# Performance work log

Hardware: AMD Instinct MI355X
Metric: run time of the kernel (lower is better)

## Reference

```python
import jax, jax.numpy as jnp
import numpy as np

B = 65536
D = 8          # model dim (hard-wired in source)
H = 2          # num_heads
A = 20         # act_size
L = 5          # tokens per embedding stream


def _attn_layer(x, Wqkv, bqkv, Wo, bo, Wl, bl):
    # x: [B, S, D]
    Bx, S, Dx = x.shape
    hd = Dx // H
    qkv = x @ Wqkv.T + bqkv                      # [B, S, 3D]
    q, k, v = jnp.split(qkv, 3, axis=-1)
    def split_heads(t):
        return t.reshape(Bx, S, H, hd).transpose(0, 2, 1, 3)  # [B,H,S,hd]
    q, k, v = split_heads(q), split_heads(k), split_heads(v)
    scores = jnp.einsum('bhqd,bhkd->bhqk', q, k) * (hd ** -0.5)
    attn = jax.nn.softmax(scores, axis=-1)       # dropout inactive at eval
    o = jnp.einsum('bhqk,bhkd->bhqd', attn, v)
    o = o.transpose(0, 2, 1, 3).reshape(Bx, S, Dx)
    x = x + (o @ Wo.T + bo)                      # residual after attention
    h = jax.nn.relu(x @ Wl.T + bl)               # linear + relu
    return x + h                                 # second residual


def setup_inputs() -> dict:
    key = jax.random.key(0)
    ks = jax.random.split(key, 20)
    s = 1.0 / np.sqrt(D)
    inp = {
        'dice_type': jax.random.randint(ks[0], (B, L), 0, 15),
        'dice_star': jax.random.randint(ks[1], (B, L), 0, 15),
        'summon_lvl': jax.random.randint(ks[2], (B, L), 0, 2),
        'emb_dice': jax.random.normal(ks[3], (15, D), jnp.float32),
        'emb_star': jax.random.normal(ks[4], (15, D), jnp.float32),
        'emb_btns': jax.random.normal(ks[5], (2, D), jnp.float32),
        'Wout': jax.random.normal(ks[6], (A, D), jnp.float32) * s,
        'bout': jnp.zeros((A,), jnp.float32),
    }
    for i in range(2):
        o = 7 + 5 * i
        inp[f'Wqkv{i}'] = jax.random.normal(ks[o], (3 * D, D), jnp.float32) * s
        inp[f'bqkv{i}'] = jnp.zeros((3 * D,), jnp.float32)
        inp[f'Wo{i}'] = jax.random.normal(ks[o + 1], (D, D), jnp.float32) * s
        inp[f'bo{i}'] = jnp.zeros((D,), jnp.float32)
        inp[f'Wl{i}'] = jax.random.normal(ks[o + 2], (D, D), jnp.float32) * s
        inp[f'bl{i}'] = jnp.zeros((D,), jnp.float32)
    return inp


def reference(dice_type, dice_star, summon_lvl,
              emb_dice, emb_star, emb_btns,
              Wqkv0, bqkv0, Wo0, bo0, Wl0, bl0,
              Wqkv1, bqkv1, Wo1, bo1, Wl1, bl1,
              Wout, bout):
    x = jnp.concatenate([emb_dice[dice_type],
                         emb_star[dice_star],
                         emb_btns[summon_lvl]], axis=1)  # [B, 15, D]
    x = _attn_layer(x, Wqkv0, bqkv0, Wo0, bo0, Wl0, bl0)
    x = _attn_layer(x, Wqkv1, bqkv1, Wo1, bo1, Wl1, bl1)
    x = jnp.mean(x, axis=1)                               # [B, D]
    return x @ Wout.T + bout                              # [B, A]
```

## Files before the change

### kernel.cpp

```cpp
#include <hip/hip_runtime.h>
#include <math.h>

#define EPB 16
#define BTOT 65536
#define C_SCALE 0.72134752044f

typedef _Float16 h2 __attribute__((ext_vector_type(2)));

#define WQKV1 0
#define BQKV1 96
#define WO0   108
#define BO0   140
#define WL0   144
#define BL0   176
#define WO1   180
#define BO1   212
#define WL1   216
#define BL1   248

__device__ __forceinline__ float exp2_fast(float x) {
#if defined(__has_builtin)
#if __has_builtin(__builtin_amdgcn_exp2f)
  return __builtin_amdgcn_exp2f(x);
#else
  return exp2f(x);
#endif
#else
  return exp2f(x);
#endif
}

union F4H2 { float4 f; h2 h[4]; };

__device__ __forceinline__ void mm8_h2(const h2* __restrict__ wp, int woff, int boff,
                                       const h2 in2[4], h2 out2[4])
{
#pragma unroll
  for (int c2 = 0; c2 < 4; ++c2) {
    h2 acc = wp[boff + c2];
#pragma unroll
    for (int p = 0; p < 4; ++p) {
      acc += (h2)(in2[p].x) * wp[woff + c2 * 8 + 2 * p];
      acc += (h2)(in2[p].y) * wp[woff + c2 * 8 + 2 * p + 1];
    }
    out2[c2] = acc;
  }
}

__global__ void BetterBot_setup(const float* __restrict__ Wqkv1, const float* __restrict__ bqkv1,
                                const float* __restrict__ Wo0, const float* __restrict__ bo0,
                                const float* __restrict__ Wl0, const float* __restrict__ bl0,
                                const float* __restrict__ Wo1, const float* __restrict__ bo1,
                                const float* __restrict__ Wl1, const float* __restrict__ bl1,
                                h2* __restrict__ ws)
{
  const int tid = threadIdx.x;
  if (tid < 96) {
    const int c2 = tid >> 3, j = tid & 7;
    float a = Wqkv1[(2 * c2) * 8 + j], b = Wqkv1[(2 * c2 + 1) * 8 + j];
    if (c2 < 4) { a *= C_SCALE; b *= C_SCALE; }
    ws[tid] = (h2){(_Float16)a, (_Float16)b};
  } else if (tid < 108) {
    const int c2 = tid - 96;
    float a = bqkv1[2 * c2], b = bqkv1[2 * c2 + 1];
    if (c2 < 4) { a *= C_SCALE; b *= C_SCALE; }
    ws[tid] = (h2){(_Float16)a, (_Float16)b};
  } else if (tid < 140) {
    const int k = tid - 108, c2 = k >> 3, j = k & 7;
    ws[tid] = (h2){(_Float16)Wo0[(2 * c2) * 8 + j], (_Float16)Wo0[(2 * c2 + 1) * 8 + j]};
  } else if (tid < 144) {
    const int c2 = tid - 140;
    ws[tid] = (h2){(_Float16)bo0[2 * c2], (_Float16)bo0[2 * c2 + 1]};
  } else if (tid < 176) {
    const int k = tid - 144, c2 = k >> 3, j = k & 7;
    ws[tid] = (h2){(_Float16)Wl0[(2 * c2) * 8 + j], (_Float16)Wl0[(2 * c2 + 1) * 8 + j]};
  } else if (tid < 180) {
    const int c2 = tid - 176;
    ws[tid] = (h2){(_Float16)bl0[2 * c2], (_Float16)bl0[2 * c2 + 1]};
  } else if (tid < 212) {
    const int k = tid - 180, c2 = k >> 3, j = k & 7;
    ws[tid] = (h2){(_Float16)Wo1[(2 * c2) * 8 + j], (_Float16)Wo1[(2 * c2 + 1) * 8 + j]};
  } else if (tid < 216) {
    const int c2 = tid - 212;
    ws[tid] = (h2){(_Float16)bo1[2 * c2], (_Float16)bo1[2 * c2 + 1]};
  } else if (tid < 248) {
    const int k = tid - 216, c2 = k >> 3, j = k & 7;
    ws[tid] = (h2){(_Float16)Wl1[(2 * c2) * 8 + j], (_Float16)Wl1[(2 * c2 + 1) * 8 + j]};
  } else if (tid < 252) {
    const int c2 = tid - 248;
    ws[tid] = (h2){(_Float16)bl1[2 * c2], (_Float16)bl1[2 * c2 + 1]};
  }
}

__global__ __launch_bounds__(256, 4) void BetterBot_44169443672375_kernel(
    const int* __restrict__ dice_type, const int* __restrict__ dice_star,
    const int* __restrict__ summon_lvl,
    const float* __restrict__ emb_dice, const float* __restrict__ emb_star,
    const float* __restrict__ emb_btns,
    const float* __restrict__ Wout, const float* __restrict__ bout,
    const float* __restrict__ Wqkv0, const float* __restrict__ bqkv0,
    const h2* __restrict__ wp,
    float* __restrict__ out)
{
  __shared__ __align__(16) float qkT[32][20];
  __shared__ __align__(16) h2 vT[32][4];
  __shared__ __align__(16) h2 xT[32][4];
  __shared__ h2 eT[32 * 33];
  __shared__ int idxT[EPB][16];
  __shared__ __align__(16) float kvb[EPB][15][16];

  const int tid = threadIdx.x;
  const int e = tid >> 4;
  const int t = tid & 15;
  const int ge = blockIdx.x * EPB + e;

  int myc = 0;
  if (t < 15) {
    int c;
    if (t < 5)       c = dice_type[ge * 5 + t];
    else if (t < 10) c = 15 + dice_star[ge * 5 + (t - 5)];
    else             c = 30 + summon_lvl[ge * 5 + (t - 10)];
    idxT[e][t] = c;
    myc = c;
  }
  {
    const int c = tid >> 3;
    const int l8 = tid & 7;
    const float* er;
    if (c < 15)      er = emb_dice + 8 * c;
    else if (c < 30) er = emb_star + 8 * (c - 15);
    else             er = emb_btns + 8 * (c - 30);
    const float4 r0 = ((const float4*)er)[0];
    const float4 r1 = ((const float4*)er)[1];
    float r[8] = {r0.x, r0.y, r0.z, r0.w, r1.x, r1.y, r1.z, r1.w};
    if (l8 < 4) xT[c][l8] = (h2){(_Float16)r[2 * l8], (_Float16)r[2 * l8 + 1]};
    float aq = bqkv0[l8], ak = bqkv0[8 + l8], av = bqkv0[16 + l8];
#pragma unroll
    for (int j = 0; j < 8; ++j) {
      aq = fmaf(r[j], Wqkv0[l8 * 8 + j], aq);
      ak = fmaf(r[j], Wqkv0[(8 + l8) * 8 + j], ak);
      av = fmaf(r[j], Wqkv0[(16 + l8) * 8 + j], av);
    }
    qkT[c][l8] = aq * C_SCALE;
    qkT[c][8 + l8] = ak;
    const float vn = __shfl_xor(av, 1);
    if ((l8 & 1) == 0) vT[c][l8 >> 1] = (h2){(_Float16)av, (_Float16)vn};
  }
  __syncthreads();

  {
    const int qi = tid >> 3;
    const int ki0 = (tid & 7) * 4;
    float qv[8];
#pragma unroll
    for (int j = 0; j < 8; ++j) qv[j] = qkT[qi][j];
#pragma unroll
    for (int jj = 0; jj < 4; ++jj) {
      const int ki = ki0 + jj;
      const float* kr = &qkT[ki][8];
      float s0 = qv[0] * kr[0];
      s0 = fmaf(qv[1], kr[1], s0); s0 = fmaf(qv[2], kr[2], s0); s0 = fmaf(qv[3], kr[3], s0);
      float s1 = qv[4] * kr[4];
      s1 = fmaf(qv[5], kr[5], s1); s1 = fmaf(qv[6], kr[6], s1); s1 = fmaf(qv[7], kr[7], s1);
      eT[qi * 33 + ki] = (h2){(_Float16)exp2_fast(s0), (_Float16)exp2_fast(s1)};
    }
  }
  __syncthreads();

  h2 x2[4];
  float q1f[8];
  if (t < 15) {
    F4H2 xx; xx.f = *(const float4*)(&xT[myc][0]);
#pragma unroll
    for (int p = 0; p < 4; ++p) x2[p] = xx.h[p];

    h2 o2[4] = {(h2)(_Float16)0.f, (h2)(_Float16)0.f, (h2)(_Float16)0.f, (h2)(_Float16)0.f};
    float sum0 = 0.f, sum1 = 0.f;
    const h2* myE = eT + myc * 33;
#pragma unroll
    for (int u = 0; u < 15; ++u) {
      const int uc = idxT[e][u];
      const h2 ee = myE[uc];
      F4H2 vv; vv.f = *(const float4*)(&vT[uc][0]);
      const h2 el = (h2)(ee.x);
      const h2 eh = (h2)(ee.y);
      o2[0] += el * vv.h[0];
      o2[1] += el * vv.h[1];
      o2[2] += eh * vv.h[2];
      o2[3] += eh * vv.h[3];
      sum0 += (float)ee.x;
      sum1 += (float)ee.y;
    }
    const float r0 = 1.0f / sum0, r1 = 1.0f / sum1;
    o2[0] *= (h2)(_Float16)r0; o2[1] *= (h2)(_Float16)r0;
    o2[2] *= (h2)(_Float16)r1; o2[3] *= (h2)(_Float16)r1;

    h2 y2[4], xn2[4], hh2[4];
    mm8_h2(wp, WO0, BO0, o2, y2);
#pragma unroll
    for (int p = 0; p < 4; ++p) xn2[p] = x2[p] + y2[p];
    mm8_h2(wp, WL0, BL0, xn2, hh2);
    const h2 z2 = (h2)(_Float16)0.f;
#pragma unroll
    for (int p = 0; p < 4; ++p) x2[p] = xn2[p] + __builtin_elementwise_max(hh2[p], z2);

    h2 qkv2[12];
#pragma unroll
    for (int c2 = 0; c2 < 12; ++c2) {
      h2 acc = wp[BQKV1 + c2];
#pragma unroll
      for (int p = 0; p < 4; ++p) {
        acc += (h2)(x2[p].x) * wp[WQKV1 + c2 * 8 + 2 * p];
        acc += (h2)(x2[p].y) * wp[WQKV1 + c2 * 8 + 2 * p + 1];
      }
      qkv2[c2] = acc;
    }
#pragma unroll
    for (int p = 0; p < 4; ++p) {
      q1f[2 * p] = (float)qkv2[p].x;
      q1f[2 * p + 1] = (float)qkv2[p].y;
    }
    *(float4*)(&kvb[e][t][0]) = make_float4((float)qkv2[4].x, (float)qkv2[4].y,
                                            (float)qkv2[5].x, (float)qkv2[5].y);
    *(float4*)(&kvb[e][t][4]) = make_float4((float)qkv2[6].x, (float)qkv2[6].y,
                                            (float)qkv2[7].x, (float)qkv2[7].y);
    *(float4*)(&kvb[e][t][8]) = make_float4((float)qkv2[8].x, (float)qkv2[8].y,
                                            (float)qkv2[9].x, (float)qkv2[9].y);
    *(float4*)(&kvb[e][t][12]) = make_float4((float)qkv2[10].x, (float)qkv2[10].y,
                                             (float)qkv2[11].x, (float)qkv2[11].y);
  }
  __syncthreads();

  float xo[8] = {0.f, 0.f, 0.f, 0.f, 0.f, 0.f, 0.f, 0.f};
  if (t < 15) {
    float o[8] = {0.f, 0.f, 0.f, 0.f, 0.f, 0.f, 0.f, 0.f};
    float sum0 = 0.f, sum1 = 0.f;
#pragma unroll
    for (int u = 0; u < 15; ++u) {
      const float4 ka = *(const float4*)(&kvb[e][u][0]);
      const float4 kb2 = *(const float4*)(&kvb[e][u][4]);
      const float4 va = *(const float4*)(&kvb[e][u][8]);
      const float4 vb2 = *(const float4*)(&kvb[e][u][12]);
      float s0 = q1f[0] * ka.x;
      s0 = fmaf(q1f[1], ka.y, s0); s0 = fmaf(q1f[2], ka.z, s0); s0 = fmaf(q1f[3], ka.w, s0);
      float s1 = q1f[4] * kb2.x;
      s1 = fmaf(q1f[5], kb2.y, s1); s1 = fmaf(q1f[6], kb2.z, s1); s1 = fmaf(q1f[7], kb2.w, s1);
      const float e0 = exp2_fast(s0);
      const float e1 = exp2_fast(s1);
      sum0 += e0; sum1 += e1;
      o[0] = fmaf(e0, va.x, o[0]); o[1] = fmaf(e0, va.y, o[1]);
      o[2] = fmaf(e0, va.z, o[2]); o[3] = fmaf(e0, va.w, o[3]);
      o[4] = fmaf(e1, vb2.x, o[4]); o[5] = fmaf(e1, vb2.y, o[5]);
      o[6] = fmaf(e1, vb2.z, o[6]); o[7] = fmaf(e1, vb2.w, o[7]);
    }
    const float r0 = 1.0f / sum0, r1 = 1.0f / sum1;
    h2 po2[4];
    po2[0] = (h2){(_Float16)(o[0] * r0), (_Float16)(o[1] * r0)};
    po2[1] = (h2){(_Float16)(o[2] * r0), (_Float16)(o[3] * r0)};
    po2[2] = (h2){(_Float16)(o[4] * r1), (_Float16)(o[5] * r1)};
    po2[3] = (h2){(_Float16)(o[6] * r1), (_Float16)(o[7] * r1)};

    h2 y2[4], xn2[4], hh2[4];
    mm8_h2(wp, WO1, BO1, po2, y2);
#pragma unroll
    for (int p = 0; p < 4; ++p) xn2[p] = x2[p] + y2[p];
    mm8_h2(wp, WL1, BL1, xn2, hh2);
    const h2 z2 = (h2)(_Float16)0.f;
#pragma unroll
    for (int p = 0; p < 4; ++p) {
      const h2 xf = xn2[p] + __builtin_elementwise_max(hh2[p], z2);
      xo[2 * p] = (float)xf.x;
      xo[2 * p + 1] = (float)xf.y;
    }
  }

  float p[8];
#pragma unroll
  for (int j = 0; j < 8; ++j) p[j] = xo[j];
#pragma unroll
  for (int j = 0; j < 8; ++j) p[j] += __shfl_xor(p[j], 1);
#pragma unroll
  for (int j = 0; j < 8; ++j) p[j] += __shfl_xor(p[j], 2);
#pragma unroll
  for (int j = 0; j < 8; ++j) p[j] += __shfl_xor(p[j], 4);
#pragma unroll
  for (int j = 0; j < 8; ++j) p[j] += __shfl_xor(p[j], 8);
  float mean[8];
#pragma unroll
  for (int j = 0; j < 8; ++j) mean[j] = p[j] * (1.0f / 15.0f);

  const int obase = ge * 20;
  {
    float acc = bout[t];
#pragma unroll
    for (int j = 0; j < 8; ++j) acc = fmaf(mean[j], Wout[t * 8 + j], acc);
    out[obase + t] = acc;
  }
  if (t < 4) {
    const int a = 16 + t;
    float acc = bout[a];
#pragma unroll
    for (int j = 0; j < 8; ++j) acc = fmaf(mean[j], Wout[a * 8 + j], acc);
    out[obase + a] = acc;
  }
}

extern "C" void kernel_launch(void* const* d_in, const int* in_sizes, int n_in,
                              void* d_out, int out_size, void* d_ws, size_t ws_size,
                              hipStream_t stream) {
  const int*   dice_type  = (const int*)d_in[0];
  const int*   dice_star  = (const int*)d_in[1];
  const int*   summon_lvl = (const int*)d_in[2];
  const float* emb_dice   = (const float*)d_in[3];
  const float* emb_star   = (const float*)d_in[4];
  const float* emb_btns   = (const float*)d_in[5];
  const float* Wout       = (const float*)d_in[6];
  const float* bout       = (const float*)d_in[7];
  const float* Wqkv0      = (const float*)d_in[8];
  const float* bqkv0      = (const float*)d_in[9];
  const float* Wo0        = (const float*)d_in[10];
  const float* bo0        = (const float*)d_in[11];
  const float* Wl0        = (const float*)d_in[12];
  const float* bl0        = (const float*)d_in[13];
  const float* Wqkv1      = (const float*)d_in[14];
  const float* bqkv1      = (const float*)d_in[15];
  const float* Wo1        = (const float*)d_in[16];
  const float* bo1        = (const float*)d_in[17];
  const float* Wl1        = (const float*)d_in[18];
  const float* bl1        = (const float*)d_in[19];
  float* out = (float*)d_out;
  h2* ws = (h2*)d_ws;

  hipLaunchKernelGGL(BetterBot_setup, dim3(1), dim3(256), 0, stream,
                     Wqkv1, bqkv1, Wo0, bo0, Wl0, bl0, Wo1, bo1, Wl1, bl1, ws);
  hipLaunchKernelGGL(BetterBot_44169443672375_kernel, dim3(BTOT / EPB), dim3(256), 0, stream,
                     dice_type, dice_star, summon_lvl,
                     emb_dice, emb_star, emb_btns, Wout, bout,
                     Wqkv0, bqkv0, (const h2*)ws, out);
}
```

Before: 131.0 us.

## Use fp16 dot2, packed conversions and head-interleaved layouts in attention

```diff
diff --git a/kernel.cpp b/kernel.cpp
--- a/kernel.cpp
+++ b/kernel.cpp
@@ -6,6 +6,7 @@
 #define C_SCALE 0.72134752044f
 
 typedef _Float16 h2 __attribute__((ext_vector_type(2)));
+typedef __fp16 fp16v2 __attribute__((ext_vector_type(2)));
 
 #define WQKV1 0
 #define BQKV1 96
@@ -17,16 +18,20 @@
 #define BO1   212
 #define WL1   216
 #define BL1   248
-
-__device__ __forceinline__ float exp2_fast(float x) {
-#if defined(__has_builtin)
-#if __has_builtin(__builtin_amdgcn_exp2f)
-  return __builtin_amdgcn_exp2f(x);
+#define WV1P  256
+#define BV1F  288
+
+__device__ __forceinline__ float exp2_fast(float x) { return __builtin_amdgcn_exp2f(x); }
+__device__ __forceinline__ float rcp_fast(float x)  { return __builtin_amdgcn_rcpf(x); }
+__device__ __forceinline__ h2 pkrtz(float a, float b) {
+  fp16v2 r = __builtin_amdgcn_cvt_pkrtz(a, b);
+  return __builtin_bit_cast(h2, r);
+}
+__device__ __forceinline__ float fdot2f(h2 a, h2 b, float c) {
+#if defined(__has_builtin) && __has_builtin(__builtin_amdgcn_fdot2)
+  return __builtin_amdgcn_fdot2(a, b, c, false);
 #else
-  return exp2f(x);
-#endif
-#else
-  return exp2f(x);
+  return (float)a.x * (float)b.x + (float)a.y * (float)b.y + c;
 #endif
 }
 
@@ -57,42 +62,57 @@
   const int tid = threadIdx.x;
   if (tid < 96) {
     const int c2 = tid >> 3, j = tid & 7;
-    float a = Wqkv1[(2 * c2) * 8 + j], b = Wqkv1[(2 * c2 + 1) * 8 + j];
-    if (c2 < 4) { a *= C_SCALE; b *= C_SCALE; }
-    ws[tid] = (h2){(_Float16)a, (_Float16)b};
+    int ra, rb; float s = 1.0f;
+    if (c2 < 4)      { ra = 2 * c2; rb = ra + 1; s = C_SCALE; }
+    else if (c2 < 8) { ra = 8 + 2 * (c2 - 4); rb = ra + 1; }
+    else             { ra = 16 + (c2 - 8); rb = ra + 4; }
+    ws[tid] = pkrtz(Wqkv1[ra * 8 + j] * s, Wqkv1[rb * 8 + j] * s);
   } else if (tid < 108) {
     const int c2 = tid - 96;
-    float a = bqkv1[2 * c2], b = bqkv1[2 * c2 + 1];
-    if (c2 < 4) { a *= C_SCALE; b *= C_SCALE; }
-    ws[tid] = (h2){(_Float16)a, (_Float16)b};
+    int ra, rb; float s = 1.0f;
+    if (c2 < 4)      { ra = 2 * c2; rb = ra + 1; s = C_SCALE; }
+    else if (c2 < 8) { ra = 8 + 2 * (c2 - 4); rb = ra + 1; }
+    else             { ra = 16 + (c2 - 8); rb = ra + 4; }
+    ws[tid] = pkrtz(bqkv1[ra] * s, bqkv1[rb] * s);
   } else if (tid < 140) {
-    const int k = tid - 108, c2 = k >> 3, j = k & 7;
-    ws[tid] = (h2){(_Float16)Wo0[(2 * c2) * 8 + j], (_Float16)Wo0[(2 * c2 + 1) * 8 + j]};
+    const int k = tid - 108, c2 = k >> 3, j = k & 7, p = j >> 1;
+    const int col = (j & 1) ? (p + 4) : p;
+    ws[tid] = pkrtz(Wo0[(2 * c2) * 8 + col], Wo0[(2 * c2 + 1) * 8 + col]);
   } else if (tid < 144) {
     const int c2 = tid - 140;
-    ws[tid] = (h2){(_Float16)bo0[2 * c2], (_Float16)bo0[2 * c2 + 1]};
+    ws[tid] = pkrtz(bo0[2 * c2], bo0[2 * c2 + 1]);
   } else if (tid < 176) {
     const int k = tid - 144, c2 = k >> 3, j = k & 7;
-    ws[tid] = (h2){(_Float16)Wl0[(2 * c2) * 8 + j], (_Float16)Wl0[(2 * c2 + 1) * 8 + j]};
+    ws[tid] = pkrtz(Wl0[(2 * c2) * 8 + j], Wl0[(2 * c2 + 1) * 8 + j]);
   } else if (tid < 180) {
     const int c2 = tid - 176;
-    ws[tid] = (h2){(_Float16)bl0[2 * c2], (_Float16)bl0[2 * c2 + 1]};
+    ws[tid] = pkrtz(bl0[2 * c2], bl0[2 * c2 + 1]);
   } else if (tid < 212) {
-    const int k = tid - 180, c2 = k >> 3, j = k & 7;
-    ws[tid] = (h2){(_Float16)Wo1[(2 * c2) * 8 + j], (_Float16)Wo1[(2 * c2 + 1) * 8 + j]};
+    const int k = tid - 180, c2 = k >> 3, j = k & 7, p = j >> 1;
+    const int col = (j & 1) ? (p + 4) : p;
+    ws[tid] = pkrtz(Wo1[(2 * c2) * 8 + col], Wo1[(2 * c2 + 1) * 8 + col]);
   } else if (tid < 216) {
     const int c2 = tid - 212;
-    ws[tid] = (h2){(_Float16)bo1[2 * c2], (_Float16)bo1[2 * c2 + 1]};
+    ws[tid] = pkrtz(bo1[2 * c2], bo1[2 * c2 + 1]);
   } else if (tid < 248) {
     const int k = tid - 216, c2 = k >> 3, j = k & 7;
-    ws[tid] = (h2){(_Float16)Wl1[(2 * c2) * 8 + j], (_Float16)Wl1[(2 * c2 + 1) * 8 + j]};
+    ws[tid] = pkrtz(Wl1[(2 * c2) * 8 + j], Wl1[(2 * c2 + 1) * 8 + j]);
   } else if (tid < 252) {
     const int c2 = tid - 248;
-    ws[tid] = (h2){(_Float16)bl1[2 * c2], (_Float16)bl1[2 * c2 + 1]};
-  }
-}
-
-__global__ __launch_bounds__(256, 4) void BetterBot_44169443672375_kernel(
+    ws[tid] = pkrtz(bl1[2 * c2], bl1[2 * c2 + 1]);
+  }
+  if (tid < 32) {
+    const int r = tid >> 2, p = tid & 3;
+    const int row = 16 + (r >> 1) + (r & 1) * 4;
+    ws[WV1P + tid] = pkrtz(Wqkv1[row * 8 + 2 * p], Wqkv1[row * 8 + 2 * p + 1]);
+  } else if (tid < 40) {
+    const int r = tid - 32;
+    const int row = 16 + (r >> 1) + (r & 1) * 4;
+    ((float*)(ws + BV1F))[r] = bqkv1[row];
+  }
+}
+
+__global__ __launch_bounds__(256, 8) void BetterBot_44169443672375_kernel(
     const int* __restrict__ dice_type, const int* __restrict__ dice_star,
     const int* __restrict__ summon_lvl,
     const float* __restrict__ emb_dice, const float* __restrict__ emb_star,
@@ -102,17 +122,19 @@
     const h2* __restrict__ wp,
     float* __restrict__ out)
 {
-  __shared__ __align__(16) float qkT[32][20];
+  __shared__ __align__(16) h2 qT16[32][4];
+  __shared__ __align__(16) h2 kT16[32][4];
   __shared__ __align__(16) h2 vT[32][4];
   __shared__ __align__(16) h2 xT[32][4];
   __shared__ h2 eT[32 * 33];
   __shared__ int idxT[EPB][16];
-  __shared__ __align__(16) float kvb[EPB][15][16];
+  __shared__ __align__(16) float kvb[EPB][15][12];
 
   const int tid = threadIdx.x;
   const int e = tid >> 4;
   const int t = tid & 15;
   const int ge = blockIdx.x * EPB + e;
+  const float* wsf = (const float*)(wp + BV1F);
 
   int myc = 0;
   if (t < 15) {
@@ -133,7 +155,7 @@
     const float4 r0 = ((const float4*)er)[0];
     const float4 r1 = ((const float4*)er)[1];
     float r[8] = {r0.x, r0.y, r0.z, r0.w, r1.x, r1.y, r1.z, r1.w};
-    if (l8 < 4) xT[c][l8] = (h2){(_Float16)r[2 * l8], (_Float16)r[2 * l8 + 1]};
+    if (l8 < 4) xT[c][l8] = pkrtz(r[2 * l8], r[2 * l8 + 1]);
     float aq = bqkv0[l8], ak = bqkv0[8 + l8], av = bqkv0[16 + l8];
 #pragma unroll
     for (int j = 0; j < 8; ++j) {
@@ -141,34 +163,37 @@
       ak = fmaf(r[j], Wqkv0[(8 + l8) * 8 + j], ak);
       av = fmaf(r[j], Wqkv0[(16 + l8) * 8 + j], av);
     }
-    qkT[c][l8] = aq * C_SCALE;
-    qkT[c][8 + l8] = ak;
-    const float vn = __shfl_xor(av, 1);
-    if ((l8 & 1) == 0) vT[c][l8 >> 1] = (h2){(_Float16)av, (_Float16)vn};
+    aq *= C_SCALE;
+    const float aq_p = __shfl_xor(aq, 1);
+    const float ak_p = __shfl_xor(ak, 1);
+    const float av_p = __shfl_xor(av, 4);
+    if ((l8 & 1) == 0) {
+      qT16[c][l8 >> 1] = pkrtz(aq, aq_p);
+      kT16[c][l8 >> 1] = pkrtz(ak, ak_p);
+    }
+    if (l8 < 4) vT[c][l8] = pkrtz(av, av_p);
   }
   __syncthreads();
 
   {
     const int qi = tid >> 3;
-    const int ki0 = (tid & 7) * 4;
-    float qv[8];
-#pragma unroll
-    for (int j = 0; j < 8; ++j) qv[j] = qkT[qi][j];
+    const int l8 = tid & 7;
+    F4H2 qr; qr.f = *(const float4*)(&qT16[qi][0]);
 #pragma unroll
     for (int jj = 0; jj < 4; ++jj) {
-      const int ki = ki0 + jj;
-      const float* kr = &qkT[ki][8];
-      float s0 = qv[0] * kr[0];
-      s0 = fmaf(qv[1], kr[1], s0); s0 = fmaf(qv[2], kr[2], s0); s0 = fmaf(qv[3], kr[3], s0);
-      float s1 = qv[4] * kr[4];
-      s1 = fmaf(qv[5], kr[5], s1); s1 = fmaf(qv[6], kr[6], s1); s1 = fmaf(qv[7], kr[7], s1);
-      eT[qi * 33 + ki] = (h2){(_Float16)exp2_fast(s0), (_Float16)exp2_fast(s1)};
+      const int ki = l8 + 8 * jj;
+      F4H2 kr; kr.f = *(const float4*)(&kT16[ki][0]);
+      const float s0 = fdot2f(qr.h[0], kr.h[0], fdot2f(qr.h[1], kr.h[1], 0.f));
+      const float s1 = fdot2f(qr.h[2], kr.h[2], fdot2f(qr.h[3], kr.h[3], 0.f));
+      eT[qi * 33 + ki] = pkrtz(exp2_fast(s0), exp2_fast(s1));
     }
   }
   __syncthreads();
 
-  h2 x2[4];
-  float q1f[8];
+  h2 x2[4] = {(h2)(_Float16)0.f, (h2)(_Float16)0.f, (h2)(_Float16)0.f, (h2)(_Float16)0.f};
+  h2 q2[4];
+  const h2 ONE0 = {(_Float16)1.f, (_Float16)0.f};
+  const h2 ONE1 = {(_Float16)0.f, (_Float16)1.f};
   if (t < 15) {
     F4H2 xx; xx.f = *(const float4*)(&xT[myc][0]);
 #pragma unroll
@@ -180,20 +205,18 @@
 #pragma unroll
     for (int u = 0; u < 15; ++u) {
       const int uc = idxT[e][u];
-      const h2 ee = myE[uc];
+      const h2 ee2 = myE[uc];
       F4H2 vv; vv.f = *(const float4*)(&vT[uc][0]);
-      const h2 el = (h2)(ee.x);
-      const h2 eh = (h2)(ee.y);
-      o2[0] += el * vv.h[0];
-      o2[1] += el * vv.h[1];
-      o2[2] += eh * vv.h[2];
-      o2[3] += eh * vv.h[3];
-      sum0 += (float)ee.x;
-      sum1 += (float)ee.y;
-    }
-    const float r0 = 1.0f / sum0, r1 = 1.0f / sum1;
-    o2[0] *= (h2)(_Float16)r0; o2[1] *= (h2)(_Float16)r0;
-    o2[2] *= (h2)(_Float16)r1; o2[3] *= (h2)(_Float16)r1;
+      sum0 = fdot2f(ee2, ONE0, sum0);
+      sum1 = fdot2f(ee2, ONE1, sum1);
+      o2[0] += ee2 * vv.h[0];
+      o2[1] += ee2 * vv.h[1];
+      o2[2] += ee2 * vv.h[2];
+      o2[3] += ee2 * vv.h[3];
+    }
+    const h2 rp2 = pkrtz(rcp_fast(sum0), rcp_fast(sum1));
+#pragma unroll
+    for (int p = 0; p < 4; ++p) o2[p] *= rp2;
 
     h2 y2[4], xn2[4], hh2[4];
     mm8_h2(wp, WO0, BO0, o2, y2);
@@ -204,9 +227,9 @@
 #pragma unroll
     for (int p = 0; p < 4; ++p) x2[p] = xn2[p] + __builtin_elementwise_max(hh2[p], z2);
 
-    h2 qkv2[12];
-#pragma unroll
-    for (int c2 = 0; c2 < 12; ++c2) {
+    h2 qkv2[8];
+#pragma unroll
+    for (int c2 = 0; c2 < 8; ++c2) {
       h2 acc = wp[BQKV1 + c2];
 #pragma unroll
       for (int p = 0; p < 4; ++p) {
@@ -216,49 +239,46 @@
       qkv2[c2] = acc;
     }
 #pragma unroll
-    for (int p = 0; p < 4; ++p) {
-      q1f[2 * p] = (float)qkv2[p].x;
-      q1f[2 * p + 1] = (float)qkv2[p].y;
-    }
-    *(float4*)(&kvb[e][t][0]) = make_float4((float)qkv2[4].x, (float)qkv2[4].y,
-                                            (float)qkv2[5].x, (float)qkv2[5].y);
-    *(float4*)(&kvb[e][t][4]) = make_float4((float)qkv2[6].x, (float)qkv2[6].y,
-                                            (float)qkv2[7].x, (float)qkv2[7].y);
-    *(float4*)(&kvb[e][t][8]) = make_float4((float)qkv2[8].x, (float)qkv2[8].y,
-                                            (float)qkv2[9].x, (float)qkv2[9].y);
-    *(float4*)(&kvb[e][t][12]) = make_float4((float)qkv2[10].x, (float)qkv2[10].y,
-                                             (float)qkv2[11].x, (float)qkv2[11].y);
+    for (int p = 0; p < 4; ++p) q2[p] = qkv2[p];
+    float vv[8];
+#pragma unroll
+    for (int r = 0; r < 8; ++r) {
+      float acc = wsf[r];
+#pragma unroll
+      for (int p = 0; p < 4; ++p) acc = fdot2f(x2[p], wp[WV1P + r * 4 + p], acc);
+      vv[r] = acc;
+    }
+    F4H2 ka;
+#pragma unroll
+    for (int p = 0; p < 4; ++p) ka.h[p] = qkv2[4 + p];
+    *(float4*)(&kvb[e][t][0]) = ka.f;
+    *(float4*)(&kvb[e][t][4]) = make_float4(vv[0], vv[1], vv[2], vv[3]);
+    *(float4*)(&kvb[e][t][8]) = make_float4(vv[4], vv[5], vv[6], vv[7]);
   }
   __syncthreads();
 
-  float xo[8] = {0.f, 0.f, 0.f, 0.f, 0.f, 0.f, 0.f, 0.f};
   if (t < 15) {
     float o[8] = {0.f, 0.f, 0.f, 0.f, 0.f, 0.f, 0.f, 0.f};
     float sum0 = 0.f, sum1 = 0.f;
 #pragma unroll
     for (int u = 0; u < 15; ++u) {
-      const float4 ka = *(const float4*)(&kvb[e][u][0]);
-      const float4 kb2 = *(const float4*)(&kvb[e][u][4]);
-      const float4 va = *(const float4*)(&kvb[e][u][8]);
-      const float4 vb2 = *(const float4*)(&kvb[e][u][12]);
-      float s0 = q1f[0] * ka.x;
-      s0 = fmaf(q1f[1], ka.y, s0); s0 = fmaf(q1f[2], ka.z, s0); s0 = fmaf(q1f[3], ka.w, s0);
-      float s1 = q1f[4] * kb2.x;
-      s1 = fmaf(q1f[5], kb2.y, s1); s1 = fmaf(q1f[6], kb2.z, s1); s1 = fmaf(q1f[7], kb2.w, s1);
+      F4H2 kk; kk.f = *(const float4*)(&kvb[e][u][0]);
+      const float4 va = *(const float4*)(&kvb[e][u][4]);
+      const float4 vb = *(const float4*)(&kvb[e][u][8]);
+      const float s0 = fdot2f(q2[0], kk.h[0], fdot2f(q2[1], kk.h[1], 0.f));
+      const float s1 = fdot2f(q2[2], kk.h[2], fdot2f(q2[3], kk.h[3], 0.f));
       const float e0 = exp2_fast(s0);
       const float e1 = exp2_fast(s1);
       sum0 += e0; sum1 += e1;
-      o[0] = fmaf(e0, va.x, o[0]); o[1] = fmaf(e0, va.y, o[1]);
-      o[2] = fmaf(e0, va.z, o[2]); o[3] = fmaf(e0, va.w, o[3]);
-      o[4] = fmaf(e1, vb2.x, o[4]); o[5] = fmaf(e1, vb2.y, o[5]);
-      o[6] = fmaf(e1, vb2.z, o[6]); o[7] = fmaf(e1, vb2.w, o[7]);
-    }
-    const float r0 = 1.0f / sum0, r1 = 1.0f / sum1;
+      o[0] = fmaf(e0, va.x, o[0]); o[1] = fmaf(e1, va.y, o[1]);
+      o[2] = fmaf(e0, va.z, o[2]); o[3] = fmaf(e1, va.w, o[3]);
+      o[4] = fmaf(e0, vb.x, o[4]); o[5] = fmaf(e1, vb.y, o[5]);
+      o[6] = fmaf(e0, vb.z, o[6]); o[7] = fmaf(e1, vb.w, o[7]);
+    }
+    const float r0 = rcp_fast(sum0), r1 = rcp_fast(sum1);
     h2 po2[4];
-    po2[0] = (h2){(_Float16)(o[0] * r0), (_Float16)(o[1] * r0)};
-    po2[1] = (h2){(_Float16)(o[2] * r0), (_Float16)(o[3] * r0)};
-    po2[2] = (h2){(_Float16)(o[4] * r1), (_Float16)(o[5] * r1)};
-    po2[3] = (h2){(_Float16)(o[6] * r1), (_Float16)(o[7] * r1)};
+#pragma unroll
+    for (int i = 0; i < 4; ++i) po2[i] = pkrtz(o[2 * i] * r0, o[2 * i + 1] * r1);
 
     h2 y2[4], xn2[4], hh2[4];
     mm8_h2(wp, WO1, BO1, po2, y2);
@@ -267,16 +287,15 @@
     mm8_h2(wp, WL1, BL1, xn2, hh2);
     const h2 z2 = (h2)(_Float16)0.f;
 #pragma unroll
-    for (int p = 0; p < 4; ++p) {
-      const h2 xf = xn2[p] + __builtin_elementwise_max(hh2[p], z2);
-      xo[2 * p] = (float)xf.x;
-      xo[2 * p + 1] = (float)xf.y;
-    }
+    for (int p = 0; p < 4; ++p) x2[p] = xn2[p] + __builtin_elementwise_max(hh2[p], z2);
+  } else {
+#pragma unroll
+    for (int p = 0; p < 4; ++p) x2[p] = (h2)(_Float16)0.f;
   }
 
   float p[8];
 #pragma unroll
-  for (int j = 0; j < 8; ++j) p[j] = xo[j];
+  for (int i = 0; i < 4; ++i) { p[2 * i] = (float)x2[i].x; p[2 * i + 1] = (float)x2[i].y; }
 #pragma unroll
   for (int j = 0; j < 8; ++j) p[j] += __shfl_xor(p[j], 1);
 #pragma unroll
```

Measured after the change: 126.9 us. 3.1% less time.
